# Optimization experiments

Measured on AMD Instinct MI355X. Metric: run time of the kernel, lower is better.

The kernel has to match this reference:

```python
import jax, jax.numpy as jnp
import numpy as np

D_MODEL = 1024
H = 16
D_K = D_MODEL // H


def setup_inputs() -> dict:
    key = jax.random.key(0)
    ks = jax.random.split(key, 12)
    B, S = 2, 2048
    scale = 1.0 / np.sqrt(D_MODEL)
    inp = {
        "q": jax.random.normal(ks[0], (B, S, D_MODEL), jnp.float32),
        "k": jax.random.normal(ks[1], (B, S, D_MODEL), jnp.float32),
        "v": jax.random.normal(ks[2], (B, S, D_MODEL), jnp.float32),
        "mask": jnp.ones((B, 1, S, S), jnp.int32),
        "w_q": jax.random.normal(ks[3], (D_MODEL, D_MODEL), jnp.float32) * scale,
        "b_q": jnp.zeros((D_MODEL,), jnp.float32),
        "w_k": jax.random.normal(ks[4], (D_MODEL, D_MODEL), jnp.float32) * scale,
        "b_k": jnp.zeros((D_MODEL,), jnp.float32),
        "w_v": jax.random.normal(ks[5], (D_MODEL, D_MODEL), jnp.float32) * scale,
        "b_v": jnp.zeros((D_MODEL,), jnp.float32),
        "w_o": jax.random.normal(ks[6], (D_MODEL, D_MODEL), jnp.float32) * scale,
        "b_o": jnp.zeros((D_MODEL,), jnp.float32),
    }
    return inp


def _split_heads(x):
    B, S, _ = x.shape
    return x.reshape(B, S, H, D_K).transpose(0, 2, 1, 3)  # [B,H,S,Dk]


def reference(q, k, v, mask, w_q, b_q, w_k, b_k, w_v, b_v, w_o, b_o):
    # Linear projections (torch Linear: x @ W^T + b)
    query = _split_heads(q @ w_q.T + b_q)
    key = _split_heads(k @ w_k.T + b_k)
    value = _split_heads(v @ w_v.T + b_v)

    # scaled dot-product attention: [B,H,S,S]
    scores = jnp.einsum("bhqd,bhkd->bhqk", query, key) / jnp.sqrt(
        jnp.asarray(D_K, query.dtype)
    )
    scores = jnp.where(mask == 0, jnp.asarray(-1e9, scores.dtype), scores)
    attn = jax.nn.softmax(scores, axis=-1)  # dropout p=0.0 -> identity
    out = jnp.einsum("bhqk,bhkd->bhqd", attn, value)  # [B,H,S,Dk]

    # combine heads -> [B,S,D_MODEL]
    B = out.shape[0]
    out = out.transpose(0, 2, 1, 3).reshape(B, -1, D_MODEL)
    return out @ w_o.T + b_o
```

## Files before the change

### kernel.cpp

```cpp
#include <hip/hip_runtime.h>
#include <hip/hip_bf16.h>

#define S_LEN 2048
#define BATCH 2
#define NH    16
#define DK    64
#define DM    1024

typedef __bf16 bf16x8 __attribute__((ext_vector_type(8)));
typedef float  f32x4  __attribute__((ext_vector_type(4)));
typedef ushort u16x8  __attribute__((ext_vector_type(8)));

__device__ __forceinline__ float bf2f(ushort u) {
    union { unsigned int i; float f; } v; v.i = ((unsigned int)u) << 16; return v.f;
}
__device__ __forceinline__ ushort f2bf(float f) {
    union { float f; unsigned int i; } v; v.f = f;
    unsigned int u = v.i;
    unsigned int r = u + 0x7fff + ((u >> 16) & 1);
    return (ushort)(r >> 16);
}
__device__ __forceinline__ unsigned int packbf(float a, float b) {
    union { float f; unsigned int u; } x, y; x.f = a; y.f = b;
    return (x.u >> 16) | (y.u & 0xFFFF0000u);
}

__device__ __forceinline__ void async_copy16(const ushort* g, ushort* l) {
    __builtin_amdgcn_global_load_lds(
        (__attribute__((address_space(1))) void*)(g),
        (__attribute__((address_space(3))) void*)(l), 16, 0, 0);
}

__global__ void detect(const ushort* __restrict__ q, int* __restrict__ flags) {
    __shared__ int red[256];
    int tid = threadIdx.x;
    int cnt = 0;
    for (int i = tid; i < 2048; i += 256) {
        ushort e = q[2 * i];
        int ex = (e >> 7) & 0xFF;
        if (ex == 0 || (ex >= 107 && ex <= 147)) cnt++;
    }
    red[tid] = cnt;
    __syncthreads();
    for (int s = 128; s > 0; s >>= 1) {
        if (tid < s) red[tid] += red[tid + s];
        __syncthreads();
    }
    if (tid == 0) {
        flags[0] = (red[0] < 1229) ? 1 : 0;
        flags[1] = 0;
    }
}

__global__ void mask_check(const int* __restrict__ mask, int* __restrict__ flags) {
    const int total = BATCH * S_LEN * S_LEN / 4;
    int idx = blockIdx.x * blockDim.x + threadIdx.x;
    int stride = gridDim.x * blockDim.x;
    bool bad = false;
    for (int i = idx; i < total; i += stride) {
        int4 v = ((const int4*)mask)[i];
        if (v.x == 0 || v.y == 0 || v.z == 0 || v.w == 0) bad = true;
    }
    if (__any(bad)) {
        if ((threadIdx.x & 63) == 0) atomicOr(&flags[1], 1);
    }
}

#define NJOBS 11
struct CvtJobs { const void* src[NJOBS]; };

__device__ __constant__ const int g_cum[NJOBS + 1] = {
    0, 4194304, 8388608, 12582912, 13631488, 14680064, 15728640,
    16777216, 16778240, 16779264, 16780288, 16781312
};

__global__ __launch_bounds__(256) void convert_all(CvtJobs J, ushort* __restrict__ conv,
                                                   const int* __restrict__ flags) {
    bool isf32 = flags[0] != 0;
    const int total_chunks = 16781312 / 8;
    int c = blockIdx.x * blockDim.x + threadIdx.x;
    int stride = gridDim.x * blockDim.x;
    for (; c < total_chunks; c += stride) {
        int e = c * 8;
        int j = 0;
        while (j + 1 < NJOBS + 1 && e >= g_cum[j + 1]) j++;
        int local = e - g_cum[j];
        if (isf32) {
            const float* s = (const float*)J.src[j] + local;
            f32x4 a = *(const f32x4*)s;
            f32x4 b = *(const f32x4*)(s + 4);
            ushort o[8] = { f2bf(a[0]), f2bf(a[1]), f2bf(a[2]), f2bf(a[3]),
                            f2bf(b[0]), f2bf(b[1]), f2bf(b[2]), f2bf(b[3]) };
            *(ushort4*)&conv[e]     = *(ushort4*)&o[0];
            *(ushort4*)&conv[e + 4] = *(ushort4*)&o[4];
        } else {
            const ushort* s = (const ushort*)J.src[j] + local;
            bf16x8 v = *(const bf16x8*)s;
            *(bf16x8*)&conv[e] = v;
        }
    }
}

struct GArg { const ushort* x; const ushort* w; const ushort* bias; void* y; int split; float scale; };

__global__ __launch_bounds__(256) void gemm_bt(GArg a0, GArg a1, GArg a2,
                                               const int* __restrict__ flags) {
    GArg A = (blockIdx.z == 0) ? a0 : (blockIdx.z == 1 ? a1 : a2);
    const int K = 1024, N = 1024;
    __shared__ ushort As[2][128 * 32];
    __shared__ ushort Bs[2][128 * 32];

    int tid = threadIdx.x;
    int w = tid >> 6, lane = tid & 63;
    int wm = (w >> 1) * 64, wn = (w & 1) * 64;

    int id = blockIdx.x + 8 * blockIdx.y;
    int m0 = (id & 31) * 128;
    int n0 = (id >> 5) * 128;

    f32x4 acc[4][4] = {};

    int srow0 = w * 16 + (lane >> 2);
    int srow1 = (w + 4) * 16 + (lane >> 2);
    int schunk = ((lane & 3) ^ ((lane >> 3) & 3)) * 8;

    int fr = lane & 15;
    int qd = lane >> 4;
    int fcp = (qd ^ ((fr >> 1) & 3)) * 8;

    const ushort* xr0 = A.x + (size_t)(m0 + srow0) * K + schunk;
    const ushort* xr1 = A.x + (size_t)(m0 + srow1) * K + schunk;
    const ushort* wr0 = A.w + (size_t)(n0 + srow0) * K + schunk;
    const ushort* wr1 = A.w + (size_t)(n0 + srow1) * K + schunk;

    async_copy16(xr0, &As[0][w * 512]);
    async_copy16(xr1, &As[0][(w + 4) * 512]);
    async_copy16(wr0, &Bs[0][w * 512]);
    async_copy16(wr1, &Bs[0][(w + 4) * 512]);

    for (int k = 0; k < 32; k++) {
        __syncthreads();
        int cur = k & 1, nxt = cur ^ 1;

        bf16x8 af[4], bfr[4];
#pragma unroll
        for (int i = 0; i < 4; i++) {
            af[i]  = *(const bf16x8*)&As[cur][(wm + i * 16 + fr) * 32 + fcp];
            bfr[i] = *(const bf16x8*)&Bs[cur][(wn + i * 16 + fr) * 32 + fcp];
        }

        if (k + 1 < 32) {
            int off = (k + 1) * 32;
            async_copy16(xr0 + off, &As[nxt][w * 512]);
            async_copy16(xr1 + off, &As[nxt][(w + 4) * 512]);
            async_copy16(wr0 + off, &Bs[nxt][w * 512]);
            async_copy16(wr1 + off, &Bs[nxt][(w + 4) * 512]);
        }

#pragma unroll
        for (int i = 0; i < 4; i++)
#pragma unroll
            for (int j = 0; j < 4; j++)
                acc[i][j] = __builtin_amdgcn_mfma_f32_16x16x32_bf16(af[i], bfr[j], acc[i][j], 0, 0, 0);
    }

    bool isf32 = flags[0] != 0;
    int crow = qd * 4;
    int ccol = fr;
#pragma unroll
    for (int j = 0; j < 4; j++) {
        int n_g = n0 + wn + j * 16 + ccol;
        float bias = bf2f(A.bias[n_g]);
#pragma unroll
        for (int i = 0; i < 4; i++) {
            if (A.split == 2) {
                ushort4 o;
                o.x = f2bf((acc[i][j][0] + bias) * A.scale);
                o.y = f2bf((acc[i][j][1] + bias) * A.scale);
                o.z = f2bf((acc[i][j][2] + bias) * A.scale);
                o.w = f2bf((acc[i][j][3] + bias) * A.scale);
                int m_g0 = m0 + wm + i * 16 + crow;
                int bb = m_g0 >> 11, s = m_g0 & 2047;
                int h = n_g >> 6, d = n_g & 63;
                *(ushort4*)&((ushort*)A.y)[((size_t)(bb * NH + h) * DK + d) * S_LEN + s] = o;
            } else {
#pragma unroll
                for (int r = 0; r < 4; r++) {
                    int m_g = m0 + wm + i * 16 + crow + r;
                    float val = (acc[i][j][r] + bias) * A.scale;
                    if (A.split) {
                        int bb = m_g >> 11, s = m_g & 2047;
                        int h = n_g >> 6, d = n_g & 63;
                        ((ushort*)A.y)[((size_t)(bb * NH + h) * S_LEN + s) * DK + d] = f2bf(val);
                    } else if (isf32) {
                        ((float*)A.y)[(size_t)m_g * N + n_g] = val;
                    } else {
                        ((ushort*)A.y)[(size_t)m_g * N + n_g] = f2bf(val);
                    }
                }
            }
        }
    }
}

#define PSTR 76

__global__ __launch_bounds__(256) void attn(const ushort* __restrict__ qp,
                                            const ushort* __restrict__ kp,
                                            const ushort* __restrict__ vp,
                                            const int* __restrict__ mask,
                                            const int* __restrict__ flags,
                                            ushort* __restrict__ ctx) {
    __shared__ ushort Ks[2][64 * 64];
    __shared__ ushort Vs[2][64 * 64];
    __shared__ ushort Pb[4][32 * PSTR];

    int tid = threadIdx.x, w = tid >> 6, lane = tid & 63;
    int id = blockIdx.x + 16 * blockIdx.y;
    int bh = id & 31;
    int b = bh >> 4, h = bh & 15;
    int q0 = (id >> 5) * 128;

    const ushort* qb  = qp + (size_t)bh * S_LEN * DK;
    const ushort* kb  = kp + (size_t)bh * S_LEN * DK;
    const ushort* vtb = vp + (size_t)bh * DK * S_LEN;
    const int* mb = mask + (size_t)b * S_LEN * S_LEN;
    bool do_mask = flags[1] != 0;

    int fr = lane & 15;
    int qd = lane >> 4;

    bf16x8 qf[2][2];
#pragma unroll
    for (int rt = 0; rt < 2; rt++)
#pragma unroll
        for (int kc = 0; kc < 2; kc++)
            qf[rt][kc] = *(const bf16x8*)&qb[(size_t)(q0 + w * 32 + rt * 16 + fr) * DK + kc * 32 + qd * 8];

    bf16x8 ones;
#pragma unroll
    for (int j = 0; j < 8; j++) ones[j] = (__bf16)1.0f;

    f32x4 oacc[2][4] = {};
    f32x4 lacc[2] = {};

    int srow0 = w * 8 + (lane >> 3);
    int srow1 = (w + 4) * 8 + (lane >> 3);
    int schunk = ((lane & 7) ^ ((lane >> 3) & 7)) * 8;

    const ushort* kr0 = kb + (size_t)srow0 * DK + schunk;
    const ushort* kr1 = kb + (size_t)srow1 * DK + schunk;
    const ushort* vr0 = vtb + (size_t)srow0 * S_LEN + schunk;
    const ushort* vr1 = vtb + (size_t)srow1 * S_LEN + schunk;

    async_copy16(kr0, &Ks[0][w * 512]);
    async_copy16(kr1, &Ks[0][(w + 4) * 512]);
    async_copy16(vr0, &Vs[0][w * 512]);
    async_copy16(vr1, &Vs[0][(w + 4) * 512]);

    for (int t = 0; t < 32; t++) {
        int k0 = t * 64;
        __syncthreads();
        int cur = t & 1, nxt = cur ^ 1;

        bf16x8 kf[2][4];
#pragma unroll
        for (int kc = 0; kc < 2; kc++)
#pragma unroll
            for (int ct = 0; ct < 4; ct++)
                kf[kc][ct] = *(const bf16x8*)&Ks[cur][(ct * 16 + fr) * 64 + (((kc * 4 + qd) ^ (fr & 7)) * 8)];

        if (t + 1 < 32) {
            int koff = (t + 1) * 64;
            async_copy16(kr0 + (size_t)koff * DK, &Ks[nxt][w * 512]);
            async_copy16(kr1 + (size_t)koff * DK, &Ks[nxt][(w + 4) * 512]);
            async_copy16(vr0 + koff, &Vs[nxt][w * 512]);
            async_copy16(vr1 + koff, &Vs[nxt][(w + 4) * 512]);
        }

        f32x4 sc[2][4] = {};
        __builtin_amdgcn_s_setprio(1);
#pragma unroll
        for (int kc = 0; kc < 2; kc++)
#pragma unroll
            for (int rt = 0; rt < 2; rt++)
#pragma unroll
                for (int ct = 0; ct < 4; ct++)
                    sc[rt][ct] = __builtin_amdgcn_mfma_f32_16x16x32_bf16(kf[kc][ct], qf[rt][kc], sc[rt][ct], 0, 0, 0);
        __builtin_amdgcn_s_setprio(0);

        if (do_mask) {
#pragma unroll
            for (int rt = 0; rt < 2; rt++) {
                int qr = q0 + w * 32 + rt * 16 + fr;
                const int* mrow = &mb[(size_t)qr * S_LEN + k0];
#pragma unroll
                for (int ct = 0; ct < 4; ct++)
#pragma unroll
                    for (int r = 0; r < 4; r++)
                        if (mrow[ct * 16 + qd * 4 + r] == 0) sc[rt][ct][r] = -1e9f;
            }
        }

#pragma unroll
        for (int rt = 0; rt < 2; rt++)
#pragma unroll
            for (int ct = 0; ct < 4; ct++) {
                float p0 = __builtin_amdgcn_exp2f(sc[rt][ct][0]);
                float p1 = __builtin_amdgcn_exp2f(sc[rt][ct][1]);
                float p2 = __builtin_amdgcn_exp2f(sc[rt][ct][2]);
                float p3 = __builtin_amdgcn_exp2f(sc[rt][ct][3]);
                uint2 pk;
                pk.x = packbf(p0, p1);
                pk.y = packbf(p2, p3);
                *(uint2*)&Pb[w][(rt * 16 + fr) * PSTR + ct * 16 + qd * 4] = pk;
            }

        bf16x8 vf[2][4];
#pragma unroll
        for (int kk = 0; kk < 2; kk++)
#pragma unroll
            for (int dt = 0; dt < 4; dt++)
                vf[kk][dt] = *(const bf16x8*)&Vs[cur][(dt * 16 + fr) * 64 + (((kk * 4 + qd) ^ (fr & 7)) * 8)];

        bf16x8 pf[2][2];
#pragma unroll
        for (int kk = 0; kk < 2; kk++)
#pragma unroll
            for (int rt = 0; rt < 2; rt++)
                pf[kk][rt] = *(const bf16x8*)&Pb[w][(rt * 16 + fr) * PSTR + kk * 32 + qd * 8];

        __builtin_amdgcn_s_setprio(1);
#pragma unroll
        for (int kk = 0; kk < 2; kk++)
#pragma unroll
            for (int rt = 0; rt < 2; rt++) {
                lacc[rt] = __builtin_amdgcn_mfma_f32_16x16x32_bf16(pf[kk][rt], ones, lacc[rt], 0, 0, 0);
#pragma unroll
                for (int dt = 0; dt < 4; dt++)
                    oacc[rt][dt] = __builtin_amdgcn_mfma_f32_16x16x32_bf16(pf[kk][rt], vf[kk][dt], oacc[rt][dt], 0, 0, 0);
            }
        __builtin_amdgcn_s_setprio(0);
    }

#pragma unroll
    for (int rt = 0; rt < 2; rt++)
#pragma unroll
        for (int r = 0; r < 4; r++) {
            float inv = 1.0f / lacc[rt][r];
            int qr = q0 + w * 32 + rt * 16 + qd * 4 + r;
            size_t rowbase = ((size_t)(b * S_LEN + qr) * NH + h) * DK;
#pragma unroll
            for (int dt = 0; dt < 4; dt++)
                ctx[rowbase + dt * 16 + fr] = f2bf(oacc[rt][dt][r] * inv);
        }
}

extern "C" void kernel_launch(void* const* d_in, const int* in_sizes, int n_in,
                              void* d_out, int out_size, void* d_ws, size_t ws_size,
                              hipStream_t stream) {
    const int* mask = (const int*)d_in[3];

    char* ws = (char*)d_ws;
    int*    flags = (int*)ws;
    ushort* conv  = (ushort*)(ws + 4096);
    const size_t conv_bytes = 16781312ull * 2;
    char* p = ws + 4096 + ((conv_bytes + 4095) & ~4095ull);
    size_t sz = (size_t)BATCH * NH * S_LEN * DK * sizeof(ushort);
    ushort* qp  = (ushort*)(p);
    ushort* kp  = (ushort*)(p + sz);
    ushort* vp  = (ushort*)(p + 2 * sz);
    ushort* ctx = (ushort*)(p + 3 * sz);

    ushort* qc  = conv + 0;
    ushort* kc  = conv + 4194304;
    ushort* vc  = conv + 8388608;
    ushort* wqc = conv + 12582912;
    ushort* wkc = conv + 13631488;
    ushort* wvc = conv + 14680064;
    ushort* woc = conv + 15728640;
    ushort* bqc = conv + 16777216;
    ushort* bkc = conv + 16778240;
    ushort* bvc = conv + 16779264;
    ushort* boc = conv + 16780288;

    detect<<<1, 256, 0, stream>>>((const ushort*)d_in[0], flags);
    mask_check<<<1024, 256, 0, stream>>>(mask, flags);

    CvtJobs J;
    J.src[0] = d_in[0];  J.src[1] = d_in[1];  J.src[2] = d_in[2];
    J.src[3] = d_in[4];  J.src[4] = d_in[6];  J.src[5] = d_in[8];
    J.src[6] = d_in[10]; J.src[7] = d_in[5];  J.src[8] = d_in[7];
    J.src[9] = d_in[9];  J.src[10] = d_in[11];
    convert_all<<<2048, 256, 0, stream>>>(J, conv, flags);

    const float cs = 0.125f * 1.44269504f;
    GArg aq{qc, wqc, bqc, qp, 1, cs};
    GArg ak{kc, wkc, bkc, kp, 1, 1.0f};
    GArg av{vc, wvc, bvc, vp, 2, 1.0f};
    gemm_bt<<<dim3(8, 32, 3), 256, 0, stream>>>(aq, ak, av, flags);

    attn<<<dim3(16, 32), 256, 0, stream>>>(qp, kp, vp, mask, flags, ctx);

    GArg ao{ctx, woc, boc, d_out, 0, 1.0f};
    gemm_bt<<<dim3(8, 32, 1), 256, 0, stream>>>(ao, ao, ao, flags);
}
```

Before: 271.5 us.

## Split attention block across eight waves with 16 query rows each

The attention kernel now launches 512 threads (8 waves) per block, each wave owning 16 query rows instead of 32. The K/V tile loads are spread over twice as many waves, and the async prefetch of the next tile is issued before the current tile's LDS fragment reads. This is meant to raise occupancy and latency hiding by lowering per-wave register pressure. In exchange each wave reuses every K/V fragment read from LDS for only half as many MFMAs, which raises LDS traffic.

```diff
diff --git a/kernel.cpp b/kernel.cpp
--- a/kernel.cpp
+++ b/kernel.cpp
@@ -205,15 +205,15 @@
 
 #define PSTR 76
 
-__global__ __launch_bounds__(256) void attn(const ushort* __restrict__ qp,
-                                            const ushort* __restrict__ kp,
-                                            const ushort* __restrict__ vp,
-                                            const int* __restrict__ mask,
-                                            const int* __restrict__ flags,
-                                            ushort* __restrict__ ctx) {
+__global__ __launch_bounds__(512, 4) void attn(const ushort* __restrict__ qp,
+                                               const ushort* __restrict__ kp,
+                                               const ushort* __restrict__ vp,
+                                               const int* __restrict__ mask,
+                                               const int* __restrict__ flags,
+                                               ushort* __restrict__ ctx) {
     __shared__ ushort Ks[2][64 * 64];
     __shared__ ushort Vs[2][64 * 64];
-    __shared__ ushort Pb[4][32 * PSTR];
+    __shared__ ushort Pb[8][16 * PSTR];
 
     int tid = threadIdx.x, w = tid >> 6, lane = tid & 63;
     int id = blockIdx.x + 16 * blockIdx.y;
@@ -230,39 +230,38 @@
     int fr = lane & 15;
     int qd = lane >> 4;
 
-    bf16x8 qf[2][2];
-#pragma unroll
-    for (int rt = 0; rt < 2; rt++)
-#pragma unroll
-        for (int kc = 0; kc < 2; kc++)
-            qf[rt][kc] = *(const bf16x8*)&qb[(size_t)(q0 + w * 32 + rt * 16 + fr) * DK + kc * 32 + qd * 8];
+    bf16x8 qf[2];
+#pragma unroll
+    for (int kc = 0; kc < 2; kc++)
+        qf[kc] = *(const bf16x8*)&qb[(size_t)(q0 + w * 16 + fr) * DK + kc * 32 + qd * 8];
 
     bf16x8 ones;
 #pragma unroll
     for (int j = 0; j < 8; j++) ones[j] = (__bf16)1.0f;
 
-    f32x4 oacc[2][4] = {};
-    f32x4 lacc[2] = {};
-
-    int srow0 = w * 8 + (lane >> 3);
-    int srow1 = (w + 4) * 8 + (lane >> 3);
+    f32x4 oacc[4] = {};
+    f32x4 lacc = {};
+
+    int srow = w * 8 + (lane >> 3);
     int schunk = ((lane & 7) ^ ((lane >> 3) & 7)) * 8;
 
-    const ushort* kr0 = kb + (size_t)srow0 * DK + schunk;
-    const ushort* kr1 = kb + (size_t)srow1 * DK + schunk;
-    const ushort* vr0 = vtb + (size_t)srow0 * S_LEN + schunk;
-    const ushort* vr1 = vtb + (size_t)srow1 * S_LEN + schunk;
-
-    async_copy16(kr0, &Ks[0][w * 512]);
-    async_copy16(kr1, &Ks[0][(w + 4) * 512]);
-    async_copy16(vr0, &Vs[0][w * 512]);
-    async_copy16(vr1, &Vs[0][(w + 4) * 512]);
+    const ushort* kr = kb + (size_t)srow * DK + schunk;
+    const ushort* vr = vtb + (size_t)srow * S_LEN + schunk;
+
+    async_copy16(kr, &Ks[0][w * 512]);
+    async_copy16(vr, &Vs[0][w * 512]);
 
     for (int t = 0; t < 32; t++) {
         int k0 = t * 64;
         __syncthreads();
         int cur = t & 1, nxt = cur ^ 1;
 
+        if (t + 1 < 32) {
+            int koff = (t + 1) * 64;
+            async_copy16(kr + (size_t)koff * DK, &Ks[nxt][w * 512]);
+            async_copy16(vr + koff, &Vs[nxt][w * 512]);
+        }
+
         bf16x8 kf[2][4];
 #pragma unroll
         for (int kc = 0; kc < 2; kc++)
@@ -270,51 +269,36 @@
             for (int ct = 0; ct < 4; ct++)
                 kf[kc][ct] = *(const bf16x8*)&Ks[cur][(ct * 16 + fr) * 64 + (((kc * 4 + qd) ^ (fr & 7)) * 8)];
 
-        if (t + 1 < 32) {
-            int koff = (t + 1) * 64;
-            async_copy16(kr0 + (size_t)koff * DK, &Ks[nxt][w * 512]);
-            async_copy16(kr1 + (size_t)koff * DK, &Ks[nxt][(w + 4) * 512]);
-            async_copy16(vr0 + koff, &Vs[nxt][w * 512]);
-            async_copy16(vr1 + koff, &Vs[nxt][(w + 4) * 512]);
-        }
-
-        f32x4 sc[2][4] = {};
+        f32x4 sc[4] = {};
         __builtin_amdgcn_s_setprio(1);
 #pragma unroll
         for (int kc = 0; kc < 2; kc++)
 #pragma unroll
-            for (int rt = 0; rt < 2; rt++)
-#pragma unroll
-                for (int ct = 0; ct < 4; ct++)
-                    sc[rt][ct] = __builtin_amdgcn_mfma_f32_16x16x32_bf16(kf[kc][ct], qf[rt][kc], sc[rt][ct], 0, 0, 0);
+            for (int ct = 0; ct < 4; ct++)
+                sc[ct] = __builtin_amdgcn_mfma_f32_16x16x32_bf16(kf[kc][ct], qf[kc], sc[ct], 0, 0, 0);
         __builtin_amdgcn_s_setprio(0);
 
         if (do_mask) {
-#pragma unroll
-            for (int rt = 0; rt < 2; rt++) {
-                int qr = q0 + w * 32 + rt * 16 + fr;
-                const int* mrow = &mb[(size_t)qr * S_LEN + k0];
-#pragma unroll
-                for (int ct = 0; ct < 4; ct++)
-#pragma unroll
-                    for (int r = 0; r < 4; r++)
-                        if (mrow[ct * 16 + qd * 4 + r] == 0) sc[rt][ct][r] = -1e9f;
-            }
-        }
-
-#pragma unroll
-        for (int rt = 0; rt < 2; rt++)
-#pragma unroll
-            for (int ct = 0; ct < 4; ct++) {
-                float p0 = __builtin_amdgcn_exp2f(sc[rt][ct][0]);
-                float p1 = __builtin_amdgcn_exp2f(sc[rt][ct][1]);
-                float p2 = __builtin_amdgcn_exp2f(sc[rt][ct][2]);
-                float p3 = __builtin_amdgcn_exp2f(sc[rt][ct][3]);
-                uint2 pk;
-                pk.x = packbf(p0, p1);
-                pk.y = packbf(p2, p3);
-                *(uint2*)&Pb[w][(rt * 16 + fr) * PSTR + ct * 16 + qd * 4] = pk;
-            }
+            int qr = q0 + w * 16 + fr;
+            const int* mrow = &mb[(size_t)qr * S_LEN + k0];
+#pragma unroll
+            for (int ct = 0; ct < 4; ct++)
+#pragma unroll
+                for (int r = 0; r < 4; r++)
+                    if (mrow[ct * 16 + qd * 4 + r] == 0) sc[ct][r] = -1e9f;
+        }
+
+#pragma unroll
+        for (int ct = 0; ct < 4; ct++) {
+            float p0 = __builtin_amdgcn_exp2f(sc[ct][0]);
+            float p1 = __builtin_amdgcn_exp2f(sc[ct][1]);
+            float p2 = __builtin_amdgcn_exp2f(sc[ct][2]);
+            float p3 = __builtin_amdgcn_exp2f(sc[ct][3]);
+            uint2 pk;
+            pk.x = packbf(p0, p1);
+            pk.y = packbf(p2, p3);
+            *(uint2*)&Pb[w][fr * PSTR + ct * 16 + qd * 4] = pk;
+        }
 
         bf16x8 vf[2][4];
 #pragma unroll
@@ -323,37 +307,31 @@
             for (int dt = 0; dt < 4; dt++)
                 vf[kk][dt] = *(const bf16x8*)&Vs[cur][(dt * 16 + fr) * 64 + (((kk * 4 + qd) ^ (fr & 7)) * 8)];
 
-        bf16x8 pf[2][2];
+        bf16x8 pf[2];
 #pragma unroll
         for (int kk = 0; kk < 2; kk++)
-#pragma unroll
-            for (int rt = 0; rt < 2; rt++)
-                pf[kk][rt] = *(const bf16x8*)&Pb[w][(rt * 16 + fr) * PSTR + kk * 32 + qd * 8];
+            pf[kk] = *(const bf16x8*)&Pb[w][fr * PSTR + kk * 32 + qd * 8];
 
         __builtin_amdgcn_s_setprio(1);
 #pragma unroll
-        for (int kk = 0; kk < 2; kk++)
-#pragma unroll
-            for (int rt = 0; rt < 2; rt++) {
-                lacc[rt] = __builtin_amdgcn_mfma_f32_16x16x32_bf16(pf[kk][rt], ones, lacc[rt], 0, 0, 0);
-#pragma unroll
-                for (int dt = 0; dt < 4; dt++)
-                    oacc[rt][dt] = __builtin_amdgcn_mfma_f32_16x16x32_bf16(pf[kk][rt], vf[kk][dt], oacc[rt][dt], 0, 0, 0);
-            }
+        for (int kk = 0; kk < 2; kk++) {
+            lacc = __builtin_amdgcn_mfma_f32_16x16x32_bf16(pf[kk], ones, lacc, 0, 0, 0);
+#pragma unroll
+            for (int dt = 0; dt < 4; dt++)
+                oacc[dt] = __builtin_amdgcn_mfma_f32_16x16x32_bf16(pf[kk], vf[kk][dt], oacc[dt], 0, 0, 0);
+        }
         __builtin_amdgcn_s_setprio(0);
     }
 
 #pragma unroll
-    for (int rt = 0; rt < 2; rt++)
-#pragma unroll
-        for (int r = 0; r < 4; r++) {
-            float inv = 1.0f / lacc[rt][r];
-            int qr = q0 + w * 32 + rt * 16 + qd * 4 + r;
-            size_t rowbase = ((size_t)(b * S_LEN + qr) * NH + h) * DK;
-#pragma unroll
-            for (int dt = 0; dt < 4; dt++)
-                ctx[rowbase + dt * 16 + fr] = f2bf(oacc[rt][dt][r] * inv);
-        }
+    for (int r = 0; r < 4; r++) {
+        float inv = 1.0f / lacc[r];
+        int qr = q0 + w * 16 + qd * 4 + r;
+        size_t rowbase = ((size_t)(b * S_LEN + qr) * NH + h) * DK;
+#pragma unroll
+        for (int dt = 0; dt < 4; dt++)
+            ctx[rowbase + dt * 16 + fr] = f2bf(oacc[dt][r] * inv);
+    }
 }
 
 extern "C" void kernel_launch(void* const* d_in, const int* in_sizes, int n_in,
@@ -400,7 +378,7 @@
     GArg av{vc, wvc, bvc, vp, 2, 1.0f};
     gemm_bt<<<dim3(8, 32, 3), 256, 0, stream>>>(aq, ak, av, flags);
 
-    attn<<<dim3(16, 32), 256, 0, stream>>>(qp, kp, vp, mask, flags, ctx);
+    attn<<<dim3(16, 32), 512, 0, stream>>>(qp, kp, vp, mask, flags, ctx);
 
     GArg ao{ctx, woc, boc, d_out, 0, 1.0f};
     gemm_bt<<<dim3(8, 32, 1), 256, 0, stream>>>(ao, ao, ao, flags);
```

Result: faster. 256.8 us (-5.4%).

## Keep P in registers via transposed PV MFMA and enlarge attention blocks

Applied to the files above, without the earlier changes.

The attention kernel drops the per-wave LDS staging buffer for the probability tile. It computes O^T using 16x16x16 bf16 MFMAs whose B operand is the exp scores already held in registers, and sums the row denominators in scalar registers with a cross-lane shuffle instead of an MFMA against a ones vector. Blocks grow to 512 threads covering 256 query rows, so each K/V tile in LDS is shared by 8 waves and each thread issues one async copy per tensor instead of two. The cost is more, smaller MFMA instructions, 8-byte V reads from LDS, and higher register pressure under the launch_bounds(512,2) constraint.

```diff
diff --git a/kernel.cpp b/kernel.cpp
--- a/kernel.cpp
+++ b/kernel.cpp
@@ -10,6 +10,7 @@
 typedef __bf16 bf16x8 __attribute__((ext_vector_type(8)));
 typedef float  f32x4  __attribute__((ext_vector_type(4)));
 typedef ushort u16x8  __attribute__((ext_vector_type(8)));
+typedef short  s16x4  __attribute__((ext_vector_type(4)));
 
 __device__ __forceinline__ float bf2f(ushort u) {
     union { unsigned int i; float f; } v; v.i = ((unsigned int)u) << 16; return v.f;
@@ -23,6 +24,11 @@
 __device__ __forceinline__ unsigned int packbf(float a, float b) {
     union { float f; unsigned int u; } x, y; x.f = a; y.f = b;
     return (x.u >> 16) | (y.u & 0xFFFF0000u);
+}
+__device__ __forceinline__ float truncbf(float a) {
+    union { float f; unsigned int u; } x; x.f = a;
+    x.u &= 0xFFFF0000u;
+    return x.f;
 }
 
 __device__ __forceinline__ void async_copy16(const ushort* g, ushort* l) {
@@ -203,23 +209,20 @@
     }
 }
 
-#define PSTR 76
-
-__global__ __launch_bounds__(256) void attn(const ushort* __restrict__ qp,
-                                            const ushort* __restrict__ kp,
-                                            const ushort* __restrict__ vp,
-                                            const int* __restrict__ mask,
-                                            const int* __restrict__ flags,
-                                            ushort* __restrict__ ctx) {
+__global__ __launch_bounds__(512, 2) void attn(const ushort* __restrict__ qp,
+                                               const ushort* __restrict__ kp,
+                                               const ushort* __restrict__ vp,
+                                               const int* __restrict__ mask,
+                                               const int* __restrict__ flags,
+                                               ushort* __restrict__ ctx) {
     __shared__ ushort Ks[2][64 * 64];
     __shared__ ushort Vs[2][64 * 64];
-    __shared__ ushort Pb[4][32 * PSTR];
 
     int tid = threadIdx.x, w = tid >> 6, lane = tid & 63;
-    int id = blockIdx.x + 16 * blockIdx.y;
+    int id = blockIdx.x + 8 * blockIdx.y;
     int bh = id & 31;
     int b = bh >> 4, h = bh & 15;
-    int q0 = (id >> 5) * 128;
+    int q0 = (id >> 5) * 256;
 
     const ushort* qb  = qp + (size_t)bh * S_LEN * DK;
     const ushort* kb  = kp + (size_t)bh * S_LEN * DK;
@@ -237,46 +240,35 @@
         for (int kc = 0; kc < 2; kc++)
             qf[rt][kc] = *(const bf16x8*)&qb[(size_t)(q0 + w * 32 + rt * 16 + fr) * DK + kc * 32 + qd * 8];
 
-    bf16x8 ones;
-#pragma unroll
-    for (int j = 0; j < 8; j++) ones[j] = (__bf16)1.0f;
-
-    f32x4 oacc[2][4] = {};
-    f32x4 lacc[2] = {};
-
-    int srow0 = w * 8 + (lane >> 3);
-    int srow1 = (w + 4) * 8 + (lane >> 3);
+    f32x4 oaccT[2][4] = {};
+    float llocal[2] = {};
+
+    int srow = w * 8 + (lane >> 3);
     int schunk = ((lane & 7) ^ ((lane >> 3) & 7)) * 8;
 
-    const ushort* kr0 = kb + (size_t)srow0 * DK + schunk;
-    const ushort* kr1 = kb + (size_t)srow1 * DK + schunk;
-    const ushort* vr0 = vtb + (size_t)srow0 * S_LEN + schunk;
-    const ushort* vr1 = vtb + (size_t)srow1 * S_LEN + schunk;
-
-    async_copy16(kr0, &Ks[0][w * 512]);
-    async_copy16(kr1, &Ks[0][(w + 4) * 512]);
-    async_copy16(vr0, &Vs[0][w * 512]);
-    async_copy16(vr1, &Vs[0][(w + 4) * 512]);
+    const ushort* kr = kb + (size_t)srow * DK + schunk;
+    const ushort* vr = vtb + (size_t)srow * S_LEN + schunk;
+
+    async_copy16(kr, &Ks[0][w * 512]);
+    async_copy16(vr, &Vs[0][w * 512]);
 
     for (int t = 0; t < 32; t++) {
         int k0 = t * 64;
         __syncthreads();
         int cur = t & 1, nxt = cur ^ 1;
 
+        if (t + 1 < 32) {
+            int koff = (t + 1) * 64;
+            async_copy16(kr + (size_t)koff * DK, &Ks[nxt][w * 512]);
+            async_copy16(vr + koff, &Vs[nxt][w * 512]);
+        }
+
         bf16x8 kf[2][4];
 #pragma unroll
         for (int kc = 0; kc < 2; kc++)
 #pragma unroll
             for (int ct = 0; ct < 4; ct++)
                 kf[kc][ct] = *(const bf16x8*)&Ks[cur][(ct * 16 + fr) * 64 + (((kc * 4 + qd) ^ (fr & 7)) * 8)];
-
-        if (t + 1 < 32) {
-            int koff = (t + 1) * 64;
-            async_copy16(kr0 + (size_t)koff * DK, &Ks[nxt][w * 512]);
-            async_copy16(kr1 + (size_t)koff * DK, &Ks[nxt][(w + 4) * 512]);
-            async_copy16(vr0 + koff, &Vs[nxt][w * 512]);
-            async_copy16(vr1 + koff, &Vs[nxt][(w + 4) * 512]);
-        }
 
         f32x4 sc[2][4] = {};
         __builtin_amdgcn_s_setprio(1);
@@ -302,6 +294,7 @@
             }
         }
 
+        s16x4 pb[2][4];
 #pragma unroll
         for (int rt = 0; rt < 2; rt++)
 #pragma unroll
@@ -310,50 +303,47 @@
                 float p1 = __builtin_amdgcn_exp2f(sc[rt][ct][1]);
                 float p2 = __builtin_amdgcn_exp2f(sc[rt][ct][2]);
                 float p3 = __builtin_amdgcn_exp2f(sc[rt][ct][3]);
-                uint2 pk;
-                pk.x = packbf(p0, p1);
-                pk.y = packbf(p2, p3);
-                *(uint2*)&Pb[w][(rt * 16 + fr) * PSTR + ct * 16 + qd * 4] = pk;
+                union { unsigned int u[2]; s16x4 v; } pk;
+                pk.u[0] = packbf(p0, p1);
+                pk.u[1] = packbf(p2, p3);
+                pb[rt][ct] = pk.v;
+                llocal[rt] += (truncbf(p0) + truncbf(p1)) + (truncbf(p2) + truncbf(p3));
             }
 
-        bf16x8 vf[2][4];
-#pragma unroll
-        for (int kk = 0; kk < 2; kk++)
+        __builtin_amdgcn_s_setprio(1);
+#pragma unroll
+        for (int ct = 0; ct < 4; ct++) {
+            s16x4 va[4];
 #pragma unroll
             for (int dt = 0; dt < 4; dt++)
-                vf[kk][dt] = *(const bf16x8*)&Vs[cur][(dt * 16 + fr) * 64 + (((kk * 4 + qd) ^ (fr & 7)) * 8)];
-
-        bf16x8 pf[2][2];
-#pragma unroll
-        for (int kk = 0; kk < 2; kk++)
+                va[dt] = *(const s16x4*)&Vs[cur][(dt * 16 + fr) * 64 + (((2 * ct + (qd >> 1)) ^ (fr & 7)) * 8) + (qd & 1) * 4];
 #pragma unroll
             for (int rt = 0; rt < 2; rt++)
-                pf[kk][rt] = *(const bf16x8*)&Pb[w][(rt * 16 + fr) * PSTR + kk * 32 + qd * 8];
-
-        __builtin_amdgcn_s_setprio(1);
-#pragma unroll
-        for (int kk = 0; kk < 2; kk++)
-#pragma unroll
-            for (int rt = 0; rt < 2; rt++) {
-                lacc[rt] = __builtin_amdgcn_mfma_f32_16x16x32_bf16(pf[kk][rt], ones, lacc[rt], 0, 0, 0);
 #pragma unroll
                 for (int dt = 0; dt < 4; dt++)
-                    oacc[rt][dt] = __builtin_amdgcn_mfma_f32_16x16x32_bf16(pf[kk][rt], vf[kk][dt], oacc[rt][dt], 0, 0, 0);
-            }
+                    oaccT[rt][dt] = __builtin_amdgcn_mfma_f32_16x16x16bf16_1k(va[dt], pb[rt][ct], oaccT[rt][dt], 0, 0, 0);
+        }
         __builtin_amdgcn_s_setprio(0);
     }
 
 #pragma unroll
-    for (int rt = 0; rt < 2; rt++)
-#pragma unroll
-        for (int r = 0; r < 4; r++) {
-            float inv = 1.0f / lacc[rt][r];
-            int qr = q0 + w * 32 + rt * 16 + qd * 4 + r;
-            size_t rowbase = ((size_t)(b * S_LEN + qr) * NH + h) * DK;
-#pragma unroll
-            for (int dt = 0; dt < 4; dt++)
-                ctx[rowbase + dt * 16 + fr] = f2bf(oacc[rt][dt][r] * inv);
-        }
+    for (int rt = 0; rt < 2; rt++) {
+        float ls = llocal[rt];
+        ls += __shfl_xor(ls, 16);
+        ls += __shfl_xor(ls, 32);
+        float inv = 1.0f / ls;
+        int qr = q0 + w * 32 + rt * 16 + fr;
+        size_t rowbase = ((size_t)(b * S_LEN + qr) * NH + h) * DK;
+#pragma unroll
+        for (int dt = 0; dt < 4; dt++) {
+            ushort4 o;
+            o.x = f2bf(oaccT[rt][dt][0] * inv);
+            o.y = f2bf(oaccT[rt][dt][1] * inv);
+            o.z = f2bf(oaccT[rt][dt][2] * inv);
+            o.w = f2bf(oaccT[rt][dt][3] * inv);
+            *(ushort4*)&ctx[rowbase + dt * 16 + qd * 4] = o;
+        }
+    }
 }
 
 extern "C" void kernel_launch(void* const* d_in, const int* in_sizes, int n_in,
@@ -400,7 +390,7 @@
     GArg av{vc, wvc, bvc, vp, 2, 1.0f};
     gemm_bt<<<dim3(8, 32, 3), 256, 0, stream>>>(aq, ak, av, flags);
 
-    attn<<<dim3(16, 32), 256, 0, stream>>>(qp, kp, vp, mask, flags, ctx);
+    attn<<<dim3(8, 32), 512, 0, stream>>>(qp, kp, vp, mask, flags, ctx);
 
     GArg ao{ctx, woc, boc, d_out, 0, 1.0f};
     gemm_bt<<<dim3(8, 32, 1), 256, 0, stream>>>(ao, ao, ao, flags);
```

New measurement: 268.6 us. No clear change (-1.1%).
